# Kernel tuning notes

Hardware: AMD Instinct MI355X
Metric: run time of the kernel (lower is better)

Reference implementation:

```python
import jax, jax.numpy as jnp
import numpy as np

H = 16   # num_heads
A = 64   # attn_size
D = 1024 # dims
NEG = -1000000000.0


def setup_inputs() -> dict:
    key = jax.random.key(0)
    k1, k2, k3, k4 = jax.random.split(key, 4)
    B, S = 2, 2048
    qs = jax.random.normal(k1, (B, S, D), dtype=jnp.float32)
    mask = jax.random.randint(k2, (B, S), 0, 2, dtype=jnp.int32)
    Wqkv = jax.random.normal(k3, (D, 3 * H * A), dtype=jnp.float32) * (1.0 / np.sqrt(D))
    Wout = jax.random.normal(k4, (H * A, D), dtype=jnp.float32) * (1.0 / np.sqrt(H * A))
    bout = jnp.zeros((D,), dtype=jnp.float32)
    return {"qs": qs, "mask": mask, "Wqkv": Wqkv, "Wout": Wout, "bout": bout}


def reference(qs, mask, Wqkv, Wout, bout):
    B, S, _ = qs.shape
    qkv = qs @ Wqkv                              # [B,S,3*H*A]
    qkv = qkv.reshape(B, S, 3 * H, A)            # split axis=2 in thirds (TF layout)
    q = jnp.transpose(qkv[:, :, 0:H, :], (0, 2, 1, 3))        # [B,H,S,A]
    k = jnp.transpose(qkv[:, :, H:2 * H, :], (0, 2, 1, 3))    # [B,H,S,A]
    v = jnp.transpose(qkv[:, :, 2 * H:3 * H, :], (0, 2, 1, 3))# [B,H,S,A]
    scores = jnp.einsum('bhqa,bhka->bhqk', q, k) / jnp.sqrt(jnp.float32(A))
    m = mask[:, None, None, :]                   # [B,1,1,S] broadcast over heads, queries
    scores = jnp.where(m == 0, NEG, scores)
    probs = jax.nn.softmax(scores, axis=-1)      # dropout_prob=0 / inference -> identity
    ctx = jnp.einsum('bhqk,bhka->bhqa', probs, v)  # [B,H,S,A]
    ctx = jnp.transpose(ctx, (0, 2, 1, 3)).reshape(B, S, H * A)
    return ctx @ Wout + bout
```

## Files before the change

### kernel.cpp

```cpp
#include <hip/hip_runtime.h>
#include <stdint.h>


typedef unsigned short u16;
typedef uint32_t u32;
typedef u16   u16x4  __attribute__((ext_vector_type(4)));
typedef u16   u16x8  __attribute__((ext_vector_type(8)));
typedef __bf16 bf16x8 __attribute__((ext_vector_type(8)));
typedef float f32x4  __attribute__((ext_vector_type(4)));

#define DEV __device__ __forceinline__

DEV u16 cvt_bf(float f) {
    return __builtin_bit_cast(u16, (__bf16)f);
}

DEV void async16(const void* g, void* l) {
    __builtin_amdgcn_global_load_lds(
        reinterpret_cast<const uint32_t __attribute__((address_space(1)))*>(
            reinterpret_cast<uintptr_t>(g)),
        reinterpret_cast<uint32_t __attribute__((address_space(3)))*>(
            reinterpret_cast<uintptr_t>(l)),
        16, 0, 0);
}

DEV f32x4 mfma16(bf16x8 a, bf16x8 b, f32x4 c) {
    return __builtin_amdgcn_mfma_f32_16x16x32_bf16(a, b, c, 0, 0, 0);
}


__global__ void k_prep(const float* __restrict__ qs, u16* __restrict__ qs_bf,
                       const int* __restrict__ m, float* __restrict__ bias,
                       const float* __restrict__ Wqkv, u16* __restrict__ WqkvT,
                       const float* __restrict__ Wout, u16* __restrict__ WoutT) {
    __shared__ float t[32][33];
    int bid = blockIdx.x;
    if (bid < 4096) {
        int i = (bid * 256 + threadIdx.x) * 4;
        float4 v = *reinterpret_cast<const float4*>(qs + i);
        u16x4 o = { cvt_bf(v.x), cvt_bf(v.y), cvt_bf(v.z), cvt_bf(v.w) };
        *reinterpret_cast<u16x4*>(qs_bf + i) = o;
        return;
    }
    if (bid < 4112) {
        int i = (bid - 4096) * 256 + threadIdx.x;
        bias[i] = m[i] ? 0.0f : -1.0e9f;
        return;
    }
    const float* src; u16* dst; int R, C, bx, by;
    if (bid < 7184) { int q = bid - 4112; src = Wqkv; dst = WqkvT; R = 1024; C = 3072; bx = q % 96; by = q / 96; }
    else            { int q = bid - 7184; src = Wout; dst = WoutT; R = 1024; C = 1024; bx = q % 32; by = q / 32; }
    int c0 = bx * 32, r0 = by * 32;
    int tx = threadIdx.x & 31, ty = threadIdx.x >> 5;
#pragma unroll
    for (int i = 0; i < 4; ++i)
        t[ty + 8 * i][tx] = src[(size_t)(r0 + ty + 8 * i) * C + c0 + tx];
    __syncthreads();
#pragma unroll
    for (int i = 0; i < 4; ++i)
        dst[(size_t)(c0 + ty + 8 * i) * R + r0 + tx] = cvt_bf(t[tx][ty + 8 * i]);
}


template <int BM, int BN, bool OUT_BF16, bool HAS_BIAS>
__global__ __launch_bounds__(256, 3) void k_gemm(
    const u16* __restrict__ A, const u16* __restrict__ Bt,
    void* __restrict__ Cv, const float* __restrict__ bias,
    int M, int N, int K)
{
    constexpr int MT = BM / 32, NT = BN / 32;
    __shared__ __attribute__((aligned(16))) u16 As[2][BM * 32];
    __shared__ __attribute__((aligned(16))) u16 Bs[2][BN * 32];

    const int tid = threadIdx.x, wave = tid >> 6, lane = tid & 63;
    const int lh = lane & 15, lg = lane >> 4;
    const int nbn = N / BN;

    const int nwg = gridDim.x;
    const int q8 = nwg >> 3, r8 = nwg & 7;
    const int xcd = blockIdx.x & 7, li = blockIdx.x >> 3;
    const int wg = (xcd < r8 ? xcd * (q8 + 1) : r8 * (q8 + 1) + (xcd - r8) * q8) + li;

    const int m0 = (wg / nbn) * BM, n0 = (wg % nbn) * BN;
    const int wm = wave >> 1, wn = wave & 1;
    const int nk = K >> 5;

    auto stage = [&](int buf, int kt) {
#pragma unroll
        for (int i = 0; i < BM / 64; ++i) {
            int c = i * 256 + tid;
            int row = c >> 2, cc = c & 3;
            int sc = cc ^ (row & 3);
            async16(A + (size_t)(m0 + row) * K + kt * 32 + sc * 8, &As[buf][c * 8]);
        }
#pragma unroll
        for (int i = 0; i < BN / 64; ++i) {
            int c = i * 256 + tid;
            int row = c >> 2, cc = c & 3;
            int sc = cc ^ (row & 3);
            async16(Bt + (size_t)(n0 + row) * K + kt * 32 + sc * 8, &Bs[buf][c * 8]);
        }
    };

    f32x4 acc[MT][NT] = {};
    stage(0, 0);
    __syncthreads();
    int buf = 0;
    for (int kt = 0; kt < nk; ++kt) {
        if (kt + 1 < nk) stage(buf ^ 1, kt + 1);
        bf16x8 af[MT], bf_[NT];
#pragma unroll
        for (int mt = 0; mt < MT; ++mt) {
            int row = wm * (BM / 2) + mt * 16 + lh;
            int off = row * 32 + ((lg ^ (row & 3)) * 8);
            af[mt] = __builtin_bit_cast(bf16x8,
                     *reinterpret_cast<const u16x8*>(&As[buf][off]));
        }
#pragma unroll
        for (int nt = 0; nt < NT; ++nt) {
            int row = wn * (BN / 2) + nt * 16 + lh;
            int off = row * 32 + ((lg ^ (row & 3)) * 8);
            bf_[nt] = __builtin_bit_cast(bf16x8,
                      *reinterpret_cast<const u16x8*>(&Bs[buf][off]));
        }
        __builtin_amdgcn_s_setprio(1);
#pragma unroll
        for (int mt = 0; mt < MT; ++mt)
#pragma unroll
            for (int nt = 0; nt < NT; ++nt)
                acc[mt][nt] = mfma16(af[mt], bf_[nt], acc[mt][nt]);
        __builtin_amdgcn_s_setprio(0);
        __syncthreads();
        buf ^= 1;
    }

#pragma unroll
    for (int mt = 0; mt < MT; ++mt)
#pragma unroll
        for (int nt = 0; nt < NT; ++nt) {
            int col = n0 + wn * (BN / 2) + nt * 16 + lh;
#pragma unroll
            for (int r = 0; r < 4; ++r) {
                int row = m0 + wm * (BM / 2) + mt * 16 + 4 * lg + r;
                float v = acc[mt][nt][r];
                if (HAS_BIAS) v += bias[col];
                if (OUT_BF16) ((u16*)Cv)[(size_t)row * N + col] = cvt_bf(v);
                else          ((float*)Cv)[(size_t)row * N + col] = v;
            }
        }
}


__global__ __launch_bounds__(256, 3) void k_attn(
    const u16* __restrict__ qkv, const float* __restrict__ biasg, u16* __restrict__ ctx)
{
    __shared__ __attribute__((aligned(16))) u16 Ks[2][64 * 64];
    __shared__ __attribute__((aligned(16))) u16 Vt[2][64 * 72];
    __shared__ __attribute__((aligned(16))) u16 Ps[4 * 32 * 72];

    const int tid = threadIdx.x, wave = tid >> 6, lane = tid & 63;
    const int lh = lane & 15, lg = lane >> 4;

    const int wg = (blockIdx.x & 7) * 64 + (blockIdx.x >> 3);
    const int qt = wg & 15, bh = wg >> 4;
    const int b = bh >> 4, h = bh & 15;

    const u16* qbase = qkv + ((size_t)b * 2048 * 48 + h) * 64;
    const u16* kbase = qkv + ((size_t)b * 2048 * 48 + 16 + h) * 64;
    const u16* vbase = qkv + ((size_t)b * 2048 * 48 + 32 + h) * 64;
    const float* brow = biasg + b * 2048;

    int srow_[2], scc_[2];
#pragma unroll
    for (int i = 0; i < 2; ++i) {
        int c = (wave * 2 + i) * 64 + lane;
        srow_[i] = c >> 3; scc_[i] = c & 7;
    }

    bf16x8 qf[2][2];
#pragma unroll
    for (int mt = 0; mt < 2; ++mt) {
        int row = qt * 128 + wave * 32 + mt * 16 + lh;
        qf[mt][0] = __builtin_bit_cast(bf16x8,
            *reinterpret_cast<const u16x8*>(qbase + (size_t)row * 3072 + lg * 8));
        qf[mt][1] = __builtin_bit_cast(bf16x8,
            *reinterpret_cast<const u16x8*>(qbase + (size_t)row * 3072 + 32 + lg * 8));
    }

    f32x4 oa[2][4] = {};
    float lst[2][4] = {};

    u16* Pw = &Ps[wave * 32 * 72];

#pragma unroll
    for (int i = 0; i < 2; ++i) {
        int srow = srow_[i], scc = scc_[i];
        async16(kbase + (size_t)srow * 3072 + (scc ^ (srow & 7)) * 8, &Ks[0][(wave * 2 + i) * 512]);
        u16x8 v = *reinterpret_cast<const u16x8*>(vbase + (size_t)srow * 3072 + scc * 8);
#pragma unroll
        for (int j = 0; j < 8; ++j) Vt[0][(scc * 8 + j) * 72 + (srow ^ (scc << 3))] = v[j];
    }

    for (int kt = 0; kt < 32; ++kt) {
        __syncthreads();
        const int buf = kt & 1;
        if (kt + 1 < 32) {
#pragma unroll
            for (int i = 0; i < 2; ++i) {
                int srow = srow_[i], scc = scc_[i];
                async16(kbase + (size_t)((kt + 1) * 64 + srow) * 3072 + (scc ^ (srow & 7)) * 8,
                        &Ks[buf ^ 1][(wave * 2 + i) * 512]);
                u16x8 v = *reinterpret_cast<const u16x8*>(
                    vbase + (size_t)((kt + 1) * 64 + srow) * 3072 + scc * 8);
#pragma unroll
                for (int j = 0; j < 8; ++j)
                    Vt[buf ^ 1][(scc * 8 + j) * 72 + (srow ^ (scc << 3))] = v[j];
            }
        }

        float biasv[4];
#pragma unroll
        for (int nt = 0; nt < 4; ++nt) biasv[nt] = brow[kt * 64 + nt * 16 + lh];

        f32x4 sa[2][4] = {};
        __builtin_amdgcn_s_setprio(1);
#pragma unroll
        for (int ks = 0; ks < 2; ++ks) {
            bf16x8 kb[4];
#pragma unroll
            for (int nt = 0; nt < 4; ++nt) {
                int row = nt * 16 + lh;
                int off = row * 64 + (((ks * 4 + lg) ^ (row & 7)) << 3);
                kb[nt] = __builtin_bit_cast(bf16x8,
                         *reinterpret_cast<const u16x8*>(&Ks[buf][off]));
            }
#pragma unroll
            for (int mt = 0; mt < 2; ++mt)
#pragma unroll
                for (int nt = 0; nt < 4; ++nt)
                    sa[mt][nt] = mfma16(qf[mt][ks], kb[nt], sa[mt][nt]);
        }
        __builtin_amdgcn_s_setprio(0);

#pragma unroll
        for (int mt = 0; mt < 2; ++mt)
#pragma unroll
            for (int nt = 0; nt < 4; ++nt)
#pragma unroll
                for (int r = 0; r < 4; ++r) {
                    float e = __expf(fmaf(sa[mt][nt][r], 0.125f, biasv[nt]));
                    lst[mt][r] += e;
                    Pw[(mt * 16 + 4 * lg + r) * 72 + nt * 16 + lh] = cvt_bf(e);
                }

        __builtin_amdgcn_s_setprio(1);
#pragma unroll
        for (int ks = 0; ks < 2; ++ks) {
            bf16x8 pa[2], vb[4];
#pragma unroll
            for (int mt = 0; mt < 2; ++mt)
                pa[mt] = __builtin_bit_cast(bf16x8,
                         *reinterpret_cast<const u16x8*>(Pw + (mt * 16 + lh) * 72 + ks * 32 + lg * 8));
#pragma unroll
            for (int nt = 0; nt < 4; ++nt) {
                int col = nt * 16 + lh;
                int off = col * 72 + (((ks * 4 + lg) ^ (col >> 3)) << 3);
                vb[nt] = __builtin_bit_cast(bf16x8,
                         *reinterpret_cast<const u16x8*>(&Vt[buf][off]));
            }
#pragma unroll
            for (int mt = 0; mt < 2; ++mt)
#pragma unroll
                for (int nt = 0; nt < 4; ++nt)
                    oa[mt][nt] = mfma16(pa[mt], vb[nt], oa[mt][nt]);
        }
        __builtin_amdgcn_s_setprio(0);
    }

#pragma unroll
    for (int mt = 0; mt < 2; ++mt)
#pragma unroll
        for (int r = 0; r < 4; ++r) {
            float s = lst[mt][r];
#pragma unroll
            for (int o = 1; o < 16; o <<= 1) s += __shfl_xor(s, o);
            lst[mt][r] = 1.0f / s;
        }

#pragma unroll
    for (int mt = 0; mt < 2; ++mt)
#pragma unroll
        for (int nt = 0; nt < 4; ++nt)
#pragma unroll
            for (int r = 0; r < 4; ++r) {
                int row = qt * 128 + wave * 32 + mt * 16 + 4 * lg + r;
                ctx[(size_t)(b * 2048 + row) * 1024 + h * 64 + nt * 16 + lh] =
                    cvt_bf(oa[mt][nt][r] * lst[mt][r]);
            }
}


extern "C" void kernel_launch(void* const* d_in, const int* in_sizes, int n_in,
                              void* d_out, int out_size, void* d_ws, size_t ws_size,
                              hipStream_t stream)
{
    const float* qs   = (const float*)d_in[0];
    const int*   mask = (const int*)d_in[1];
    const float* Wqkv = (const float*)d_in[2];
    const float* Wout = (const float*)d_in[3];
    const float* bout = (const float*)d_in[4];
    float* out = (float*)d_out;

    char* ws = (char*)d_ws;
    u16*   qs_bf = (u16*)(ws);
    u16*   WqkvT = (u16*)(ws + 8388608);
    u16*   WoutT = (u16*)(ws + 14680064);
    u16*   qkvb  = (u16*)(ws + 16777216);
    u16*   ctxb  = (u16*)(ws + 41943040);
    float* biasb = (float*)(ws + 50331648);

    k_prep<<<8208, 256, 0, stream>>>(qs, qs_bf, mask, biasb, Wqkv, WqkvT, Wout, WoutT);

    k_gemm<128, 128, true, false><<<768, 256, 0, stream>>>(qs_bf, WqkvT, qkvb, nullptr, 4096, 3072, 1024);
    k_attn<<<512, 256, 0, stream>>>(qkvb, biasb, ctxb);
    k_gemm<128, 64, false, true><<<512, 256, 0, stream>>>(ctxb, WoutT, out, bout, 4096, 1024, 1024);
}
```

Baseline: 194.8 us.

## Triple-buffer GEMM LDS staging with vmcnt-based waits instead of full syncthreads

Expands the GEMM shared-memory staging from double to triple buffering, so tile kt+2 is loaded asynchronously while tile kt is computed. The full __syncthreads drain is replaced by an s_waitcnt vmcnt that only waits for the older stage's loads, followed by an s_barrier. This is meant to hide global-to-LDS latency better. The cost is more LDS per block, which could reduce occupancy under launch_bounds(256,3), and correctness now depends on the hand-set vmcnt values matching the number of loads issued per stage.

```diff
diff --git a/kernel.cpp b/kernel.cpp
--- a/kernel.cpp
+++ b/kernel.cpp
@@ -69,8 +69,9 @@
     int M, int N, int K)
 {
     constexpr int MT = BM / 32, NT = BN / 32;
-    __shared__ __attribute__((aligned(16))) u16 As[2][BM * 32];
-    __shared__ __attribute__((aligned(16))) u16 Bs[2][BN * 32];
+    constexpr int SI = BM / 64 + BN / 64;
+    __shared__ __attribute__((aligned(16))) u16 As[3][BM * 32];
+    __shared__ __attribute__((aligned(16))) u16 Bs[3][BN * 32];
 
     const int tid = threadIdx.x, wave = tid >> 6, lane = tid & 63;
     const int lh = lane & 15, lg = lane >> 4;
@@ -102,12 +103,13 @@
         }
     };
 
-    f32x4 acc[MT][NT] = {};
-    stage(0, 0);
-    __syncthreads();
-    int buf = 0;
-    for (int kt = 0; kt < nk; ++kt) {
-        if (kt + 1 < nk) stage(buf ^ 1, kt + 1);
+    auto waitcnt_si = [&]() {
+        if constexpr (SI == 4) asm volatile("s_waitcnt vmcnt(4)" ::: "memory");
+        else                   asm volatile("s_waitcnt vmcnt(3)" ::: "memory");
+        __builtin_amdgcn_sched_barrier(0);
+    };
+
+    auto compute = [&](int buf) {
         bf16x8 af[MT], bf_[NT];
 #pragma unroll
         for (int mt = 0; mt < MT; ++mt) {
@@ -123,15 +125,44 @@
             bf_[nt] = __builtin_bit_cast(bf16x8,
                       *reinterpret_cast<const u16x8*>(&Bs[buf][off]));
         }
+        return [=](f32x4 (&acc)[MT][NT]) {
+#pragma unroll
+            for (int mt = 0; mt < MT; ++mt)
+#pragma unroll
+                for (int nt = 0; nt < NT; ++nt)
+                    acc[mt][nt] = mfma16(af[mt], bf_[nt], acc[mt][nt]);
+        };
+    };
+
+    f32x4 acc[MT][NT] = {};
+
+    stage(0, 0);
+    stage(1, 1);
+    waitcnt_si();
+    __builtin_amdgcn_s_barrier();
+
+    for (int kt = 0; kt < nk - 2; ++kt) {
+        const int buf = kt % 3;
+        stage((kt + 2) % 3, kt + 2);
+        auto fma = compute(buf);
         __builtin_amdgcn_s_setprio(1);
-#pragma unroll
-        for (int mt = 0; mt < MT; ++mt)
-#pragma unroll
-            for (int nt = 0; nt < NT; ++nt)
-                acc[mt][nt] = mfma16(af[mt], bf_[nt], acc[mt][nt]);
+        fma(acc);
         __builtin_amdgcn_s_setprio(0);
-        __syncthreads();
-        buf ^= 1;
+        waitcnt_si();
+        __builtin_amdgcn_s_barrier();
+    }
+    {
+        auto fma = compute((nk - 2) % 3);
+        __builtin_amdgcn_s_setprio(1);
+        fma(acc);
+        __builtin_amdgcn_s_setprio(0);
+        asm volatile("s_waitcnt vmcnt(0)" ::: "memory");
+        __builtin_amdgcn_sched_barrier(0);
+        __builtin_amdgcn_s_barrier();
+    }
+    {
+        auto fma = compute((nk - 1) % 3);
+        fma(acc);
     }
 
 #pragma unroll
```

New measurement: 194.0 us. Within noise of the previous version (-0.4%).
